# Kernel tuning notes

Measured on AMD Instinct MI355X. Metric: run time of the kernel, lower is better.

The kernel has to match this reference:

```python
import jax, jax.numpy as jnp
import numpy as np

T, B, OBS, LAT, HID = 512, 256, 128, 64, 256


def setup_inputs() -> dict:
    key = jax.random.key(0)
    ks = jax.random.split(key, 20)
    s = 0.05
    return {
        "x": jax.random.normal(ks[0], (T, B, OBS), jnp.float32),
        "eps": jax.random.normal(ks[1], (T, B, LAT), jnp.float32),
        # GRU params (torch layout: [3H, in], gate order r,z,n)
        "W_ih": jax.random.normal(ks[2], (3 * HID, OBS), jnp.float32) * s,
        "W_hh": jax.random.normal(ks[3], (3 * HID, HID), jnp.float32) * s,
        "b_ih": jax.random.normal(ks[4], (3 * HID,), jnp.float32) * s,
        "b_hh": jax.random.normal(ks[5], (3 * HID,), jnp.float32) * s,
        # transition net
        "tW1": jax.random.normal(ks[6], (HID, LAT), jnp.float32) * s,
        "tb1": jax.random.normal(ks[7], (HID,), jnp.float32) * s,
        "tW2": jax.random.normal(ks[8], (2 * LAT, HID), jnp.float32) * s,
        "tb2": jax.random.normal(ks[9], (2 * LAT,), jnp.float32) * s,
        # posterior net
        "pW1": jax.random.normal(ks[10], (HID, HID + LAT), jnp.float32) * s,
        "pb1": jax.random.normal(ks[11], (HID,), jnp.float32) * s,
        "pW2": jax.random.normal(ks[12], (2 * LAT, HID), jnp.float32) * s,
        "pb2": jax.random.normal(ks[13], (2 * LAT,), jnp.float32) * s,
        # decoder net
        "dW1": jax.random.normal(ks[14], (HID, LAT), jnp.float32) * s,
        "db1": jax.random.normal(ks[15], (HID,), jnp.float32) * s,
        "dW2": jax.random.normal(ks[16], (OBS, HID), jnp.float32) * s,
        "db2": jax.random.normal(ks[17], (OBS,), jnp.float32) * s,
    }


def _gru(x, W_ih, W_hh, b_ih, b_hh):
    # Precompute input projections for all timesteps: [T,B,3H]
    gx = jnp.einsum("tbi,gi->tbg", x, W_ih) + b_ih
    H = W_hh.shape[1]

    def step(h, gxt):
        gh = h @ W_hh.T + b_hh
        xr, xz, xn = gxt[:, :H], gxt[:, H:2 * H], gxt[:, 2 * H:]
        hr, hz, hn = gh[:, :H], gh[:, H:2 * H], gh[:, 2 * H:]
        r = jax.nn.sigmoid(xr + hr)
        z = jax.nn.sigmoid(xz + hz)
        n = jnp.tanh(xn + r * hn)
        h_new = (1.0 - z) * n + z * h
        return h_new, h_new

    h0 = jnp.zeros((x.shape[1], H), x.dtype)
    _, hs = jax.lax.scan(step, h0, gx)
    return hs  # [T,B,H]


def reference(x, eps, W_ih, W_hh, b_ih, b_hh, tW1, tb1, tW2, tb2,
              pW1, pb1, pW2, pb2, dW1, db1, dW2, db2):
    hs = _gru(x, W_ih, W_hh, b_ih, b_hh)  # [T,B,H]
    L = tW1.shape[1]

    def step(z_prev, inp):
        h_t, eps_t = inp
        prior = jax.nn.relu(z_prev @ tW1.T + tb1) @ tW2.T + tb2
        prior_mean, prior_logvar = prior[:, :L], prior[:, L:]
        pin = jnp.concatenate([h_t, z_prev], axis=1)
        post = jax.nn.relu(pin @ pW1.T + pb1) @ pW2.T + pb2
        post_mean, post_logvar = post[:, :L], post[:, L:]
        z_t = post_mean + eps_t * jnp.exp(0.5 * post_logvar)
        x_recon = jax.nn.relu(z_t @ dW1.T + db1) @ dW2.T + db2
        return z_t, (x_recon, prior_mean, prior_logvar, post_mean, post_logvar)

    z0 = jnp.zeros((x.shape[1], L), x.dtype)
    _, outs = jax.lax.scan(step, z0, (hs, eps))
    recons, prior_mean, prior_logvar, post_mean, post_logvar = outs
    return (recons, prior_mean, prior_logvar, post_mean, post_logvar)
```

## Files before the change

kernel.cpp:

```cpp
#include <hip/hip_runtime.h>
#include <hip/hip_fp16.h>

#define TT 512
#define BB 256
#define OBS 128
#define LAT 64
#define HID 256

typedef short bvec8 __attribute__((ext_vector_type(8)));
typedef float fvec4 __attribute__((ext_vector_type(4)));
typedef _Float16 hvec8 __attribute__((ext_vector_type(8)));
typedef _Float16 hvec4 __attribute__((ext_vector_type(4)));

__device__ __forceinline__ short f2bf(float f){
  union { float f; unsigned u; } v; v.f = f;
  unsigned u = v.u;
  return (short)((u + 0x7FFFu + ((u >> 16) & 1u)) >> 16);
}

__device__ __forceinline__ bvec8 cvt8(const float* __restrict__ p){
  const float4* q = (const float4*)p;
  float4 lo = q[0], hi = q[1];
  bvec8 r;
  r[0] = f2bf(lo.x); r[1] = f2bf(lo.y); r[2] = f2bf(lo.z); r[3] = f2bf(lo.w);
  r[4] = f2bf(hi.x); r[5] = f2bf(hi.y); r[6] = f2bf(hi.z); r[7] = f2bf(hi.w);
  return r;
}

__device__ __forceinline__ fvec4 mfma16(bvec8 a, bvec8 b, fvec4 c){
  return __builtin_amdgcn_mfma_f32_16x16x32_bf16(a, b, c, 0, 0, 0);
}

__device__ __forceinline__ float fast_rcp(float x){ return __builtin_amdgcn_rcpf(x); }

__device__ __forceinline__ void lds_barrier(){
  asm volatile("s_waitcnt lgkmcnt(0)" ::: "memory");
  __builtin_amdgcn_s_barrier();
  asm volatile("" ::: "memory");
}

__global__ void cvt_kernel(const float* __restrict__ src, short* __restrict__ dst, int n){
  int i = blockIdx.x * 256 + threadIdx.x;
  if (i < n) dst[i] = f2bf(src[i]);
}

__global__ __launch_bounds__(256) void gx_kernel(
    const float* __restrict__ x, const short* __restrict__ Wih_bf,
    const float* __restrict__ b_ih, const float* __restrict__ b_hh,
    __half* __restrict__ gxrz, __half* __restrict__ gxn)
{
  const int tid  = threadIdx.x;
  const int wave = tid >> 6;
  const int lane = tid & 63;
  const int quad = lane >> 4;
  const int nl   = lane & 15;
  const int rowbase = blockIdx.x * 64 + wave * 16;
  const int rowq    = rowbase >> 4;

  bvec8 af[4];
#pragma unroll
  for (int ks = 0; ks < 4; ++ks)
    af[ks] = cvt8(x + (size_t)(rowbase + nl)*OBS + ks*32 + quad*8);

  for (int nt48 = 0; nt48 < 48; ++nt48){
    const int n = nt48*16 + nl;
    fvec4 acc = (fvec4)0.0f;
#pragma unroll
    for (int ks = 0; ks < 4; ++ks){
      bvec8 bw = *(const bvec8*)(Wih_bf + (size_t)n*OBS + ks*32 + quad*8);
      acc = mfma16(af[ks], bw, acc);
    }
    const int g   = nt48 >> 4;
    float bias = b_ih[n] + (g < 2 ? b_hh[n] : 0.0f);
    hvec4 s;
#pragma unroll
    for (int r = 0; r < 4; ++r) s[r] = (_Float16)(acc[r] + bias);
    const int wc  = (nt48 & 15) >> 1;
    const int ntc = nt48 & 1;
    const size_t tb = (size_t)rowq*512 + wc*64 + quad*16 + nl;
    if (g < 2) *(hvec4*)(gxrz + tb*16 + g*8 + ntc*4) = s;
    else       *(hvec4*)(gxn  + tb*8  + ntc*4)       = s;
  }
}

__global__ __launch_bounds__(256) void upre_kernel(
    const short* __restrict__ h_all, const short* __restrict__ Pw1,
    const float* __restrict__ pb1, __half* __restrict__ usw)
{
  const int tid  = threadIdx.x;
  const int wave = tid >> 6;
  const int lane = tid & 63;
  const int quad = lane >> 4;
  const int nl   = lane & 15;
  const int rowbase = (blockIdx.x * 4 + wave) * 32;
  const int rowq0   = rowbase >> 4;

  bvec8 af[2][8];
#pragma unroll
  for (int mt = 0; mt < 2; ++mt)
#pragma unroll
    for (int ks = 0; ks < 8; ++ks)
      af[mt][ks] = *(const bvec8*)(h_all + (size_t)(rowbase + mt*16 + nl)*HID + ks*32 + quad*8);

  for (int nt16 = 0; nt16 < 16; ++nt16){
    const int n = nt16*16 + nl;
    fvec4 acc[2];
    acc[0] = (fvec4)0.0f; acc[1] = (fvec4)0.0f;
#pragma unroll
    for (int ks = 0; ks < 8; ++ks){
      bvec8 bw = *(const bvec8*)(Pw1 + (size_t)n*320 + ks*32 + quad*8);
#pragma unroll
      for (int mt = 0; mt < 2; ++mt) acc[mt] = mfma16(af[mt][ks], bw, acc[mt]);
    }
    float bias = pb1[n];
    const int wc  = nt16 >> 1;
    const int ntc = nt16 & 1;
#pragma unroll
    for (int mt = 0; mt < 2; ++mt){
      hvec4 s;
#pragma unroll
      for (int r = 0; r < 4; ++r) s[r] = (_Float16)(acc[mt][r] + bias);
      const size_t tb = (size_t)(rowq0 + mt)*512 + wc*64 + quad*16 + nl;
      *(hvec4*)(usw + tb*8 + ntc*4) = s;
    }
  }
}

__attribute__((amdgpu_flat_work_group_size(512,512), amdgpu_waves_per_eu(2,2)))
__global__ void gru_kernel(
    const __half* __restrict__ gxrz, const __half* __restrict__ gxn,
    const short* __restrict__ Whh_bf,
    const float* __restrict__ b_hh,
    short* __restrict__ h_all)
{
  const int tid  = threadIdx.x;
  const int wave = tid >> 6;
  const int lane = tid & 63;
  const int quad = lane >> 4;
  const int nl   = lane & 15;
  const int b0   = blockIdx.x * 16;

  __shared__ __align__(16) short hA[2][16][264];
  __shared__ __align__(16) short WnL[4][2][8][512];

  bvec8 Whr[8][2], Whz[8][2], Whn[4][2];
  float bnh[2];
#pragma unroll
  for (int nt = 0; nt < 2; ++nt){
    const int j = wave*32 + nt*16 + nl;
#pragma unroll
    for (int ks = 0; ks < 8; ++ks){
      Whr[ks][nt] = *(const bvec8*)(Whh_bf + ((size_t)(0*HID + j))*HID + ks*32 + quad*8);
      Whz[ks][nt] = *(const bvec8*)(Whh_bf + ((size_t)(1*HID + j))*HID + ks*32 + quad*8);
    }
#pragma unroll
    for (int ks = 0; ks < 4; ++ks)
      Whn[ks][nt] = *(const bvec8*)(Whh_bf + ((size_t)(2*HID + j))*HID + ks*32 + quad*8);
#pragma unroll
    for (int ks = 4; ks < 8; ++ks){
      bvec8 w = *(const bvec8*)(Whh_bf + ((size_t)(2*HID + j))*HID + ks*32 + quad*8);
      *(bvec8*)&WnL[ks-4][nt][wave][lane*8] = w;
    }
    bnh[nt] = b_hh[2*HID + j];
  }

  float hreg[2][4];
#pragma unroll
  for (int nt = 0; nt < 2; ++nt)
#pragma unroll
    for (int r = 0; r < 4; ++r) hreg[nt][r] = 0.0f;

  const __half* grzp = gxrz + ((size_t)blockIdx.x*512 + tid)*16;
  const __half* gnp  = gxn  + ((size_t)blockIdx.x*512 + tid)*8;
  const size_t RZSTEP = (size_t)16*512*16;
  const size_t NSTEP  = (size_t)16*512*8;

  hvec8 grzA = *(const hvec8*)grzp;
  hvec8 grzB = *(const hvec8*)(grzp + 8);
  hvec8 gnA  = *(const hvec8*)gnp;

  const int orow = tid >> 5;
  const int oseg = tid & 31;
  lds_barrier();

  for (int i = 0; i < TT; ++i){
    if (i > 0){
      bvec8 v = *(const bvec8*)&hA[i&1][orow][oseg*8];
      *(bvec8*)(h_all + ((size_t)(i-1)*BB + b0 + orow)*HID + oseg*8) = v;
    }

    fvec4 ar[2], az[2], anh_[2];
#pragma unroll
    for (int nt = 0; nt < 2; ++nt){
#pragma unroll
      for (int r = 0; r < 4; ++r){
        ar[nt][r] = (float)grzA[nt*4+r];
        az[nt][r] = (float)grzB[nt*4+r];
      }
      anh_[nt] = (fvec4)0.0f;
    }

    if (i + 1 < TT){
      const __half* p = grzp + (size_t)(i+1)*RZSTEP;
      grzA = *(const hvec8*)p;
      grzB = *(const hvec8*)(p + 8);
    }

    if (i > 0){
#pragma unroll
      for (int ks = 0; ks < 8; ++ks){
        bvec8 a = *(const bvec8*)&hA[i&1][nl][ks*32 + quad*8];
#pragma unroll
        for (int nt = 0; nt < 2; ++nt){
          ar[nt] = mfma16(a, Whr[ks][nt], ar[nt]);
          az[nt] = mfma16(a, Whz[ks][nt], az[nt]);
          if (ks < 4){
            anh_[nt] = mfma16(a, Whn[ks][nt], anh_[nt]);
          } else {
            bvec8 w = *(const bvec8*)&WnL[ks-4][nt][wave][lane*8];
            anh_[nt] = mfma16(a, w, anh_[nt]);
          }
        }
      }
    }

#pragma unroll
    for (int nt = 0; nt < 2; ++nt){
      const int j = wave*32 + nt*16 + nl;
#pragma unroll
      for (int r = 0; r < 4; ++r){
        float rg = fast_rcp(1.0f + __expf(-ar[nt][r]));
        float zg = fast_rcp(1.0f + __expf(-az[nt][r]));
        float nx = (float)gnA[nt*4+r];
        float e2 = __expf(2.0f*(nx + rg*(anh_[nt][r] + bnh[nt])));
        float ng = 1.0f - 2.0f*fast_rcp(e2 + 1.0f);
        float hn = (1.0f - zg)*ng + zg*hreg[nt][r];
        hreg[nt][r] = hn;
        hA[(i+1)&1][quad*4 + r][j] = f2bf(hn);
      }
    }

    if (i + 1 < TT)
      gnA = *(const hvec8*)(gnp + (size_t)(i+1)*NSTEP);

    lds_barrier();
  }
  {
    bvec8 v = *(const bvec8*)&hA[TT&1][orow][oseg*8];
    *(bvec8*)(h_all + ((size_t)(TT-1)*BB + b0 + orow)*HID + oseg*8) = v;
  }
}

__global__ __launch_bounds__(512) void zscan_kernel(
    const __half* __restrict__ usw, const float* __restrict__ eps,
    const short* __restrict__ Pw1, const short* __restrict__ Pw2,
    const float* __restrict__ pb2,
    short* __restrict__ z_all,
    float* __restrict__ post_mean, float* __restrict__ post_logvar)
{
  const int tid  = threadIdx.x;
  const int wave = tid >> 6;
  const int lane = tid & 63;
  const int quad = lane >> 4;
  const int nl   = lane & 15;
  const int b0   = blockIdx.x * 16;

  __shared__ __align__(16) short zA[2][16][72];
  __shared__ __align__(16) short uA[16][264];
  __shared__ float postL[16][132];

  bvec8 W1z[2][2];
#pragma unroll
  for (int nt = 0; nt < 2; ++nt){
    const int n = wave*32 + nt*16 + nl;
#pragma unroll
    for (int ks = 0; ks < 2; ++ks)
      W1z[ks][nt] = *(const bvec8*)(Pw1 + (size_t)n*320 + 256 + ks*32 + quad*8);
  }
  bvec8 W2[8];
  {
    const int n2 = wave*16 + nl;
#pragma unroll
    for (int ks = 0; ks < 8; ++ks)
      W2[ks] = *(const bvec8*)(Pw2 + (size_t)n2*HID + ks*32 + quad*8);
  }

  const int zm  = tid >> 5;
  const int zl  = (tid & 31) * 2;
  float2 pb2m = *(const float2*)(pb2 + zl);
  float2 pb2v = *(const float2*)(pb2 + 64 + zl);

  const __half* ub = usw + ((size_t)blockIdx.x*512 + tid)*8;
  const size_t USTEP = (size_t)16*512*8;
  hvec8 upf = *(const hvec8*)ub;
  float2 ef = *(const float2*)(eps + ((size_t)0*BB + b0 + zm)*LAT + zl);

  for (int i = 0; i < TT; ++i){
    fvec4 au[2];
#pragma unroll
    for (int nt = 0; nt < 2; ++nt)
#pragma unroll
      for (int r = 0; r < 4; ++r)
        au[nt][r] = (float)upf[nt*4+r];

    if (i + 1 < TT)
      upf = *(const hvec8*)(ub + (size_t)(i+1)*USTEP);

    if (i > 0){
#pragma unroll
      for (int ks = 0; ks < 2; ++ks){
        bvec8 a = *(const bvec8*)&zA[i&1][nl][ks*32 + quad*8];
#pragma unroll
        for (int nt = 0; nt < 2; ++nt) au[nt] = mfma16(a, W1z[ks][nt], au[nt]);
      }
    }
#pragma unroll
    for (int nt = 0; nt < 2; ++nt){
      const int n = wave*32 + nt*16 + nl;
#pragma unroll
      for (int r = 0; r < 4; ++r){
        float u = au[nt][r];
        uA[quad*4 + r][n] = f2bf(u > 0.0f ? u : 0.0f);
      }
    }
    lds_barrier();

    fvec4 ap = (fvec4)0.0f;
#pragma unroll
    for (int ks = 0; ks < 8; ++ks){
      bvec8 a = *(const bvec8*)&uA[nl][ks*32 + quad*8];
      ap = mfma16(a, W2[ks], ap);
    }
    {
      const int n2 = wave*16 + nl;
#pragma unroll
      for (int r = 0; r < 4; ++r) postL[quad*4 + r][n2] = ap[r];
    }
    lds_barrier();

    {
      float m0 = postL[zm][zl+0] + pb2m.x, lv0 = postL[zm][64+zl+0] + pb2v.x;
      float m1 = postL[zm][zl+1] + pb2m.y, lv1 = postL[zm][64+zl+1] + pb2v.y;
      float z0 = m0 + ef.x * __expf(0.5f*lv0);
      float z1 = m1 + ef.y * __expf(0.5f*lv1);
      size_t orow = ((size_t)i*BB + b0 + zm)*LAT + zl;
      short2 zb; zb.x = f2bf(z0); zb.y = f2bf(z1);
      *(short2*)(z_all + orow) = zb;
      float2 mm; mm.x = m0; mm.y = m1;
      float2 vv; vv.x = lv0; vv.y = lv1;
      *(float2*)(post_mean + orow)   = mm;
      *(float2*)(post_logvar + orow) = vv;
      *(short2*)&zA[(i+1)&1][zm][zl] = zb;
      if (i + 1 < TT)
        ef = *(const float2*)(eps + ((size_t)(i+1)*BB + b0 + zm)*LAT + zl);
    }
    lds_barrier();
  }
}

__global__ __launch_bounds__(256) void tail_kernel(
    const short* __restrict__ z_all,
    const short* __restrict__ Tw1, const short* __restrict__ Tw2,
    const short* __restrict__ Dw1, const short* __restrict__ Dw2,
    const float* __restrict__ tb1, const float* __restrict__ tb2,
    const float* __restrict__ db1, const float* __restrict__ db2,
    float* __restrict__ prior_mean, float* __restrict__ prior_logvar,
    float* __restrict__ recons)
{
  const int tid  = threadIdx.x;
  const int wave = tid >> 6;
  const int lane = tid & 63;
  const int quad = lane >> 4;
  const int nl   = lane & 15;
  const int wg   = blockIdx.x;
  const int p    = wg >> 11;
  const int t    = (wg >> 2) & 511;
  const int mb   = wg & 3;

  const short* W1 = p ? Dw1 : Tw1;
  const short* W2 = p ? Dw2 : Tw2;
  const float* B1 = p ? db1 : tb1;
  const float* B2 = p ? db2 : tb2;

  __shared__ __align__(16) short u1[64][264];
  __shared__ float b1s[HID], b2s[OBS];

  b1s[tid] = B1[tid];
  if (tid < OBS) b2s[tid] = B2[tid];
  __syncthreads();

  const bool zzero = (p == 0 && t == 0);
  const int  tz    = p ? t : (t - 1);
  const short* zsrc = z_all + (((size_t)(zzero ? 0 : tz))*BB + mb*64)*LAT;

  fvec4 acc1[4][4];
  for (int a = 0; a < 4; ++a) for (int b = 0; b < 4; ++b) acc1[a][b] = (fvec4)0.0f;
  for (int ks = 0; ks < 2; ++ks){
    bvec8 af[4];
    for (int mt = 0; mt < 4; ++mt){
      if (zzero) af[mt] = (bvec8)(short)0;
      else af[mt] = *(const bvec8*)(zsrc + (mt*16 + nl)*LAT + ks*32 + quad*8);
    }
    for (int nt = 0; nt < 4; ++nt){
      int n = (wave*4 + nt)*16 + nl;
      bvec8 bw = *(const bvec8*)(W1 + n*LAT + ks*32 + quad*8);
      for (int mt = 0; mt < 4; ++mt) acc1[mt][nt] = mfma16(af[mt], bw, acc1[mt][nt]);
    }
  }
  for (int nt = 0; nt < 4; ++nt){
    int n = (wave*4 + nt)*16 + nl;
    float bias = b1s[n];
    for (int mt = 0; mt < 4; ++mt)
      for (int r = 0; r < 4; ++r){
        float v = acc1[mt][nt][r] + bias;
        u1[mt*16 + quad*4 + r][n] = f2bf(v > 0.0f ? v : 0.0f);
      }
  }
  __syncthreads();

  fvec4 acc2[4][2];
  for (int a = 0; a < 4; ++a) for (int b = 0; b < 2; ++b) acc2[a][b] = (fvec4)0.0f;
  for (int ks = 0; ks < 8; ++ks){
    bvec8 af[4];
    for (int mt = 0; mt < 4; ++mt)
      af[mt] = *(const bvec8*)(&u1[mt*16 + nl][ks*32 + quad*8]);
    for (int nt = 0; nt < 2; ++nt){
      int n = (wave*2 + nt)*16 + nl;
      bvec8 bw = *(const bvec8*)(W2 + n*HID + ks*32 + quad*8);
      for (int mt = 0; mt < 4; ++mt) acc2[mt][nt] = mfma16(af[mt], bw, acc2[mt][nt]);
    }
  }
  for (int nt = 0; nt < 2; ++nt){
    int n = (wave*2 + nt)*16 + nl;
    float bias = b2s[n];
    for (int mt = 0; mt < 4; ++mt)
      for (int r = 0; r < 4; ++r){
        int b = mb*64 + mt*16 + quad*4 + r;
        size_t row = (size_t)t*BB + b;
        float v = acc2[mt][nt][r] + bias;
        if (p) recons[row*OBS + n] = v;
        else if (n < LAT) prior_mean[row*LAT + n] = v;
        else              prior_logvar[row*LAT + (n - LAT)] = v;
      }
  }
}

extern "C" void kernel_launch(void* const* d_in, const int* in_sizes, int n_in,
                              void* d_out, int out_size, void* d_ws, size_t ws_size,
                              hipStream_t stream) {
  const float* x    = (const float*)d_in[0];
  const float* eps  = (const float*)d_in[1];
  const float* W_ih = (const float*)d_in[2];
  const float* W_hh = (const float*)d_in[3];
  const float* b_ih = (const float*)d_in[4];
  const float* b_hh = (const float*)d_in[5];
  const float* tW1  = (const float*)d_in[6];
  const float* tb1  = (const float*)d_in[7];
  const float* tW2  = (const float*)d_in[8];
  const float* tb2  = (const float*)d_in[9];
  const float* pW1  = (const float*)d_in[10];
  const float* pb1  = (const float*)d_in[11];
  const float* pW2  = (const float*)d_in[12];
  const float* pb2  = (const float*)d_in[13];
  const float* dW1  = (const float*)d_in[14];
  const float* db1  = (const float*)d_in[15];
  const float* dW2  = (const float*)d_in[16];
  const float* db2  = (const float*)d_in[17];

  float* out          = (float*)d_out;
  float* recons       = out;
  float* prior_mean   = out + 16777216;
  float* prior_logvar = out + 25165824;
  float* post_mean    = out + 33554432;
  float* post_logvar  = out + 41943040;

  char* ws = (char*)d_ws;
  short* h_all = (short*)ws;
  short* z_all = (short*)(ws + 67108864);
  short* wts   = (short*)(ws + 67108864 + 16777216);
  short* Pw1 = wts;
  short* Pw2 = Pw1 + 81920;
  short* Tw1 = Pw2 + 32768;
  short* Tw2 = Tw1 + 16384;
  short* Dw1 = Tw2 + 32768;
  short* Dw2 = Dw1 + 16384;
  short* Wih_bf = Dw2 + 32768;
  short* Whh_bf = Wih_bf + 98304;

  __half* gxrz = (__half*)d_out;
  __half* gxn  = (__half*)d_out + 67108864;
  __half* usw  = (__half*)d_out;

  cvt_kernel<<<(81920+255)/256, 256, 0, stream>>>(pW1, Pw1, 81920);
  cvt_kernel<<<(32768+255)/256, 256, 0, stream>>>(pW2, Pw2, 32768);
  cvt_kernel<<<(16384+255)/256, 256, 0, stream>>>(tW1, Tw1, 16384);
  cvt_kernel<<<(32768+255)/256, 256, 0, stream>>>(tW2, Tw2, 32768);
  cvt_kernel<<<(16384+255)/256, 256, 0, stream>>>(dW1, Dw1, 16384);
  cvt_kernel<<<(32768+255)/256, 256, 0, stream>>>(dW2, Dw2, 32768);
  cvt_kernel<<<(98304+255)/256, 256, 0, stream>>>(W_ih, Wih_bf, 98304);
  cvt_kernel<<<(196608+255)/256, 256, 0, stream>>>(W_hh, Whh_bf, 196608);

  gx_kernel<<<2048, 256, 0, stream>>>(x, Wih_bf, b_ih, b_hh, gxrz, gxn);
  gru_kernel<<<16, 512, 0, stream>>>(gxrz, gxn, Whh_bf, b_hh, h_all);
  upre_kernel<<<1024, 256, 0, stream>>>(h_all, Pw1, pb1, usw);
  zscan_kernel<<<16, 512, 0, stream>>>(usw, eps, Pw1, Pw2, pb2,
                                       z_all, post_mean, post_logvar);
  tail_kernel<<<4096, 256, 0, stream>>>(z_all, Tw1, Tw2, Dw1, Dw2,
                                        tb1, tb2, db1, db2,
                                        prior_mean, prior_logvar, recons);
}
```

Before: 1.796 ms.

## Permute K in recurrent weights so scan kernels write packed outputs directly

Result: slower. 1.900 ms (+5.8%).

```diff
diff --git a/kernel.cpp b/kernel.cpp
--- a/kernel.cpp
+++ b/kernel.cpp
@@ -16,6 +16,12 @@
   union { float f; unsigned u; } v; v.f = f;
   unsigned u = v.u;
   return (short)((u + 0x7FFFu + ((u >> 16) & 1u)) >> 16);
+}
+
+__device__ __forceinline__ unsigned cvt_pk_bf16(float lo, float hi){
+  unsigned r;
+  asm("v_cvt_pk_bf16_f32 %0, %1, %2" : "=v"(r) : "v"(lo), "v"(hi));
+  return r;
 }
 
 __device__ __forceinline__ bvec8 cvt8(const float* __restrict__ p){
@@ -42,6 +48,15 @@
 __global__ void cvt_kernel(const float* __restrict__ src, short* __restrict__ dst, int n){
   int i = blockIdx.x * 256 + threadIdx.x;
   if (i < n) dst[i] = f2bf(src[i]);
+}
+
+__global__ void cvtp_kernel(const float* __restrict__ src, short* __restrict__ dst,
+                            int K, int KP){
+  int k = blockIdx.x * 256 + threadIdx.x;
+  int row = blockIdx.y;
+  if (k >= K) return;
+  int ksrc = (k < KP) ? ((k & ~31) | ((k & 31) >> 1) | ((k & 1) << 4)) : k;
+  dst[(size_t)row*K + k] = f2bf(src[(size_t)row*K + ksrc]);
 }
 
 __global__ __launch_bounds__(256) void gx_kernel(
@@ -84,7 +99,7 @@
 }
 
 __global__ __launch_bounds__(256) void upre_kernel(
-    const short* __restrict__ h_all, const short* __restrict__ Pw1,
+    const short* __restrict__ h_all, const short* __restrict__ Pw1p,
     const float* __restrict__ pb1, __half* __restrict__ usw)
 {
   const int tid  = threadIdx.x;
@@ -108,7 +123,7 @@
     acc[0] = (fvec4)0.0f; acc[1] = (fvec4)0.0f;
 #pragma unroll
     for (int ks = 0; ks < 8; ++ks){
-      bvec8 bw = *(const bvec8*)(Pw1 + (size_t)n*320 + ks*32 + quad*8);
+      bvec8 bw = *(const bvec8*)(Pw1p + (size_t)n*320 + ks*32 + quad*8);
 #pragma unroll
       for (int mt = 0; mt < 2; ++mt) acc[mt] = mfma16(af[mt][ks], bw, acc[mt]);
     }
@@ -170,25 +185,22 @@
 #pragma unroll
     for (int r = 0; r < 4; ++r) hreg[nt][r] = 0.0f;
 
+  const size_t RZSTEP = (size_t)16*512*16;
+  const size_t NSTEP  = (size_t)16*512*8;
   const __half* grzp = gxrz + ((size_t)blockIdx.x*512 + tid)*16;
   const __half* gnp  = gxn  + ((size_t)blockIdx.x*512 + tid)*8;
-  const size_t RZSTEP = (size_t)16*512*16;
-  const size_t NSTEP  = (size_t)16*512*8;
 
   hvec8 grzA = *(const hvec8*)grzp;
   hvec8 grzB = *(const hvec8*)(grzp + 8);
   hvec8 gnA  = *(const hvec8*)gnp;
-
-  const int orow = tid >> 5;
-  const int oseg = tid & 31;
+  grzp += RZSTEP; gnp += NSTEP;
+
+  const int cc2 = wave*32 + nl*2;
+  short* hout = h_all + ((size_t)(b0 + quad*4))*HID + cc2;
+
   lds_barrier();
 
   for (int i = 0; i < TT; ++i){
-    if (i > 0){
-      bvec8 v = *(const bvec8*)&hA[i&1][orow][oseg*8];
-      *(bvec8*)(h_all + ((size_t)(i-1)*BB + b0 + orow)*HID + oseg*8) = v;
-    }
-
     fvec4 ar[2], az[2], anh_[2];
 #pragma unroll
     for (int nt = 0; nt < 2; ++nt){
@@ -197,13 +209,13 @@
         ar[nt][r] = (float)grzA[nt*4+r];
         az[nt][r] = (float)grzB[nt*4+r];
       }
-      anh_[nt] = (fvec4)0.0f;
+      anh_[nt] = (fvec4)bnh[nt];
     }
 
     if (i + 1 < TT){
-      const __half* p = grzp + (size_t)(i+1)*RZSTEP;
-      grzA = *(const hvec8*)p;
-      grzB = *(const hvec8*)(p + 8);
+      grzA = *(const hvec8*)grzp;
+      grzB = *(const hvec8*)(grzp + 8);
+      grzp += RZSTEP;
     }
 
     if (i > 0){
@@ -225,35 +237,37 @@
     }
 
 #pragma unroll
-    for (int nt = 0; nt < 2; ++nt){
-      const int j = wave*32 + nt*16 + nl;
-#pragma unroll
-      for (int r = 0; r < 4; ++r){
-        float rg = fast_rcp(1.0f + __expf(-ar[nt][r]));
-        float zg = fast_rcp(1.0f + __expf(-az[nt][r]));
-        float nx = (float)gnA[nt*4+r];
-        float e2 = __expf(2.0f*(nx + rg*(anh_[nt][r] + bnh[nt])));
-        float ng = 1.0f - 2.0f*fast_rcp(e2 + 1.0f);
-        float hn = (1.0f - zg)*ng + zg*hreg[nt][r];
-        hreg[nt][r] = hn;
-        hA[(i+1)&1][quad*4 + r][j] = f2bf(hn);
-      }
-    }
-
-    if (i + 1 < TT)
-      gnA = *(const hvec8*)(gnp + (size_t)(i+1)*NSTEP);
+    for (int rr = 0; rr < 4; ++rr){
+      float rg0 = fast_rcp(1.0f + __expf(-ar[0][rr]));
+      float zg0 = fast_rcp(1.0f + __expf(-az[0][rr]));
+      float ng0 = 1.0f - 2.0f*fast_rcp(__expf(2.0f*((float)gnA[rr] + rg0*anh_[0][rr])) + 1.0f);
+      float h0  = ng0 + zg0*(hreg[0][rr] - ng0);
+      hreg[0][rr] = h0;
+
+      float rg1 = fast_rcp(1.0f + __expf(-ar[1][rr]));
+      float zg1 = fast_rcp(1.0f + __expf(-az[1][rr]));
+      float ng1 = 1.0f - 2.0f*fast_rcp(__expf(2.0f*((float)gnA[4+rr] + rg1*anh_[1][rr])) + 1.0f);
+      float h1  = ng1 + zg1*(hreg[1][rr] - ng1);
+      hreg[1][rr] = h1;
+
+      unsigned pk = cvt_pk_bf16(h0, h1);
+      *(unsigned*)&hA[(i+1)&1][quad*4 + rr][cc2] = pk;
+      *(unsigned*)(hout + (size_t)rr*HID) = pk;
+    }
+    hout += (size_t)BB*HID;
+
+    if (i + 1 < TT){
+      gnA = *(const hvec8*)gnp;
+      gnp += NSTEP;
+    }
 
     lds_barrier();
-  }
-  {
-    bvec8 v = *(const bvec8*)&hA[TT&1][orow][oseg*8];
-    *(bvec8*)(h_all + ((size_t)(TT-1)*BB + b0 + orow)*HID + oseg*8) = v;
   }
 }
 
 __global__ __launch_bounds__(512) void zscan_kernel(
     const __half* __restrict__ usw, const float* __restrict__ eps,
-    const short* __restrict__ Pw1, const short* __restrict__ Pw2,
+    const short* __restrict__ Pw1p, const short* __restrict__ Pw2p,
     const float* __restrict__ pb2,
     short* __restrict__ z_all,
     float* __restrict__ post_mean, float* __restrict__ post_logvar)
@@ -267,7 +281,6 @@
 
   __shared__ __align__(16) short zA[2][16][72];
   __shared__ __align__(16) short uA[16][264];
-  __shared__ float postL[16][132];
 
   bvec8 W1z[2][2];
 #pragma unroll
@@ -275,25 +288,42 @@
     const int n = wave*32 + nt*16 + nl;
 #pragma unroll
     for (int ks = 0; ks < 2; ++ks)
-      W1z[ks][nt] = *(const bvec8*)(Pw1 + (size_t)n*320 + 256 + ks*32 + quad*8);
-  }
-  bvec8 W2[8];
-  {
-    const int n2 = wave*16 + nl;
-#pragma unroll
-    for (int ks = 0; ks < 8; ++ks)
-      W2[ks] = *(const bvec8*)(Pw2 + (size_t)n2*HID + ks*32 + quad*8);
-  }
-
-  const int zm  = tid >> 5;
-  const int zl  = (tid & 31) * 2;
-  float2 pb2m = *(const float2*)(pb2 + zl);
-  float2 pb2v = *(const float2*)(pb2 + 64 + zl);
-
+      W1z[ks][nt] = *(const bvec8*)(Pw1p + (size_t)n*320 + 256 + ks*32 + quad*8);
+  }
+
+  bvec8 W2[8][2];
+  float pb2m = 0.0f, pb2v = 0.0f;
+  const int c = wave*16 + nl;
+  if (wave < 4){
+#pragma unroll
+    for (int nt2 = 0; nt2 < 2; ++nt2){
+      const int n2 = nt2*64 + c;
+#pragma unroll
+      for (int ks = 0; ks < 8; ++ks)
+        W2[ks][nt2] = *(const bvec8*)(Pw2p + (size_t)n2*HID + ks*32 + quad*8);
+    }
+    pb2m = pb2[c];
+    pb2v = pb2[64 + c];
+  }
+
+  const size_t USTEP = (size_t)16*512*8;
   const __half* ub = usw + ((size_t)blockIdx.x*512 + tid)*8;
-  const size_t USTEP = (size_t)16*512*8;
   hvec8 upf = *(const hvec8*)ub;
-  float2 ef = *(const float2*)(eps + ((size_t)0*BB + b0 + zm)*LAT + zl);
+  ub += USTEP;
+
+  const float* epsb = eps + ((size_t)(b0 + quad*4))*LAT + c;
+  float*  pmb = post_mean   + ((size_t)(b0 + quad*4))*LAT + c;
+  float*  pvb = post_logvar + ((size_t)(b0 + quad*4))*LAT + c;
+  short*  zob = z_all       + ((size_t)(b0 + quad*4))*LAT + c;
+
+  float ef[4];
+  if (wave < 4){
+#pragma unroll
+    for (int rr = 0; rr < 4; ++rr) ef[rr] = epsb[rr*LAT];
+    epsb += (size_t)BB*LAT;
+  }
+
+  const int cc2u = wave*32 + nl*2;
 
   for (int i = 0; i < TT; ++i){
     fvec4 au[2];
@@ -303,8 +333,10 @@
       for (int r = 0; r < 4; ++r)
         au[nt][r] = (float)upf[nt*4+r];
 
-    if (i + 1 < TT)
-      upf = *(const hvec8*)(ub + (size_t)(i+1)*USTEP);
+    if (i + 1 < TT){
+      upf = *(const hvec8*)ub;
+      ub += USTEP;
+    }
 
     if (i > 0){
 #pragma unroll
@@ -315,44 +347,39 @@
       }
     }
 #pragma unroll
-    for (int nt = 0; nt < 2; ++nt){
-      const int n = wave*32 + nt*16 + nl;
-#pragma unroll
-      for (int r = 0; r < 4; ++r){
-        float u = au[nt][r];
-        uA[quad*4 + r][n] = f2bf(u > 0.0f ? u : 0.0f);
-      }
+    for (int r = 0; r < 4; ++r){
+      float u0 = au[0][r] > 0.0f ? au[0][r] : 0.0f;
+      float u1 = au[1][r] > 0.0f ? au[1][r] : 0.0f;
+      *(unsigned*)&uA[quad*4 + r][cc2u] = cvt_pk_bf16(u0, u1);
     }
     lds_barrier();
 
-    fvec4 ap = (fvec4)0.0f;
-#pragma unroll
-    for (int ks = 0; ks < 8; ++ks){
-      bvec8 a = *(const bvec8*)&uA[nl][ks*32 + quad*8];
-      ap = mfma16(a, W2[ks], ap);
-    }
-    {
-      const int n2 = wave*16 + nl;
-#pragma unroll
-      for (int r = 0; r < 4; ++r) postL[quad*4 + r][n2] = ap[r];
-    }
-    lds_barrier();
-
-    {
-      float m0 = postL[zm][zl+0] + pb2m.x, lv0 = postL[zm][64+zl+0] + pb2v.x;
-      float m1 = postL[zm][zl+1] + pb2m.y, lv1 = postL[zm][64+zl+1] + pb2v.y;
-      float z0 = m0 + ef.x * __expf(0.5f*lv0);
-      float z1 = m1 + ef.y * __expf(0.5f*lv1);
-      size_t orow = ((size_t)i*BB + b0 + zm)*LAT + zl;
-      short2 zb; zb.x = f2bf(z0); zb.y = f2bf(z1);
-      *(short2*)(z_all + orow) = zb;
-      float2 mm; mm.x = m0; mm.y = m1;
-      float2 vv; vv.x = lv0; vv.y = lv1;
-      *(float2*)(post_mean + orow)   = mm;
-      *(float2*)(post_logvar + orow) = vv;
-      *(short2*)&zA[(i+1)&1][zm][zl] = zb;
-      if (i + 1 < TT)
-        ef = *(const float2*)(eps + ((size_t)(i+1)*BB + b0 + zm)*LAT + zl);
+    if (wave < 4){
+      fvec4 ap[2];
+      ap[0] = (fvec4)0.0f; ap[1] = (fvec4)0.0f;
+#pragma unroll
+      for (int ks = 0; ks < 8; ++ks){
+        bvec8 a = *(const bvec8*)&uA[nl][ks*32 + quad*8];
+        ap[0] = mfma16(a, W2[ks][0], ap[0]);
+        ap[1] = mfma16(a, W2[ks][1], ap[1]);
+      }
+#pragma unroll
+      for (int rr = 0; rr < 4; ++rr){
+        float mean = ap[0][rr] + pb2m;
+        float lv   = ap[1][rr] + pb2v;
+        float z    = mean + ef[rr]*__expf(0.5f*lv);
+        short zb   = f2bf(z);
+        pmb[rr*LAT] = mean;
+        pvb[rr*LAT] = lv;
+        zob[rr*LAT] = zb;
+        zA[(i+1)&1][quad*4 + rr][c] = zb;
+      }
+      pmb += (size_t)BB*LAT; pvb += (size_t)BB*LAT; zob += (size_t)BB*LAT;
+      if (i + 1 < TT){
+#pragma unroll
+        for (int rr = 0; rr < 4; ++rr) ef[rr] = epsb[rr*LAT];
+        epsb += (size_t)BB*LAT;
+      }
     }
     lds_barrier();
   }
@@ -491,14 +518,14 @@
   __half* gxn  = (__half*)d_out + 67108864;
   __half* usw  = (__half*)d_out;
 
-  cvt_kernel<<<(81920+255)/256, 256, 0, stream>>>(pW1, Pw1, 81920);
-  cvt_kernel<<<(32768+255)/256, 256, 0, stream>>>(pW2, Pw2, 32768);
+  cvtp_kernel<<<dim3(2,256), 256, 0, stream>>>(pW1, Pw1, 320, 256);
+  cvtp_kernel<<<dim3(1,128), 256, 0, stream>>>(pW2, Pw2, 256, 256);
+  cvtp_kernel<<<dim3(1,768), 256, 0, stream>>>(W_hh, Whh_bf, 256, 256);
   cvt_kernel<<<(16384+255)/256, 256, 0, stream>>>(tW1, Tw1, 16384);
   cvt_kernel<<<(32768+255)/256, 256, 0, stream>>>(tW2, Tw2, 32768);
   cvt_kernel<<<(16384+255)/256, 256, 0, stream>>>(dW1, Dw1, 16384);
   cvt_kernel<<<(32768+255)/256, 256, 0, stream>>>(dW2, Dw2, 32768);
   cvt_kernel<<<(98304+255)/256, 256, 0, stream>>>(W_ih, Wih_bf, 98304);
-  cvt_kernel<<<(196608+255)/256, 256, 0, stream>>>(W_hh, Whh_bf, 196608);
 
   gx_kernel<<<2048, 256, 0, stream>>>(x, Wih_bf, b_ih, b_hh, gxrz, gxn);
   gru_kernel<<<16, 512, 0, stream>>>(gxrz, gxn, Whh_bf, b_hh, h_all);
```
